# Optimization experiments

Measured on AMD Instinct MI355X. Metric: run time of the kernel, lower is better.

## Reference

```python
import jax, jax.numpy as jnp
import numpy as np

B, S, H = 2, 2048, 1024
NQ, NKV, HD, RANK = 16, 4, 64, 8
THETA = 10000.0
LORA_SCALE = 16 / RANK  # alpha / rank = 2.0
ATTN_SCALE = 1.0 / np.sqrt(HD)


def setup_inputs() -> dict:
    key = jax.random.key(0)
    ks = jax.random.split(key, 14)
    n = lambda k, shape, s: jax.random.normal(k, shape, jnp.float32) * s
    return {
        "x": n(ks[0], (B, S, H), 1.0),
        # nn.Linear weights: [out_features, in_features], y = x @ W.T (scaled small for stability)
        "Wq": n(ks[1], (NQ * HD, H), 0.02),
        "Wk": n(ks[2], (NKV * HD, H), 0.02),
        "Wv": n(ks[3], (NKV * HD, H), 0.02),
        "Wo": n(ks[4], (H, NQ * HD), 0.02),
        "qA": n(ks[5], (RANK, H), 0.05), "qB": n(ks[6], (NQ * HD, RANK), 0.05),
        "kA": n(ks[7], (RANK, H), 0.05), "kB": n(ks[8], (NKV * HD, RANK), 0.05),
        "vA": n(ks[9], (RANK, H), 0.05), "vB": n(ks[10], (NKV * HD, RANK), 0.05),
        "oA": n(ks[11], (RANK, NQ * HD), 0.05), "oB": n(ks[12], (H, RANK), 0.05),
    }


def _lora_proj(x, W, A, Bm):
    # x @ W.T + ((x @ A.T) @ B.T) * lora_scaling
    return x @ W.T + ((x @ A.T) @ Bm.T) * LORA_SCALE


def _rope(x, cos_h, sin_h):
    # x: [b, h, s, d]; even/odd interleaved split, concatenated output (matches torch ref)
    x1, x2 = x[..., ::2], x[..., 1::2]
    return jnp.concatenate([x1 * cos_h - x2 * sin_h, x1 * sin_h + x2 * cos_h], axis=-1)


def _forward(x, Wq, Wk, Wv, Wo, qA, qB, kA, kB, vA, vB, oA, oB):
    b, s, _ = x.shape
    q = _lora_proj(x, Wq, qA, qB).reshape(b, s, NQ, HD).transpose(0, 2, 1, 3)
    k = _lora_proj(x, Wk, kA, kB).reshape(b, s, NKV, HD).transpose(0, 2, 1, 3)
    v = _lora_proj(x, Wv, vA, vB).reshape(b, s, NKV, HD).transpose(0, 2, 1, 3)

    inv_freq = 1.0 / (THETA ** (jnp.arange(0, HD, 2, dtype=jnp.float32) / HD))  # [HD/2]
    freqs = jnp.arange(s, dtype=jnp.float32)[:, None] * inv_freq[None, :]  # [s, HD/2]
    cos_h = jnp.cos(freqs)[None, None]  # [1,1,s,HD/2]
    sin_h = jnp.sin(freqs)[None, None]
    q = _rope(q, cos_h, sin_h)
    k = _rope(k, cos_h, sin_h)

    rep = NQ // NKV  # GQA: repeat_interleave along head axis
    k = jnp.repeat(k, rep, axis=1)
    v = jnp.repeat(v, rep, axis=1)

    attn = jax.nn.softmax(jnp.einsum('bhqd,bhkd->bhqk', q, k) * ATTN_SCALE, axis=-1)
    out = jnp.einsum('bhqk,bhkd->bhqd', attn, v)
    out = out.transpose(0, 2, 1, 3).reshape(b, s, NQ * HD)
    return _lora_proj(out, Wo, oA, oB)


def reference(x, Wq, Wk, Wv, Wo, qA, qB, kA, kB, vA, vB, oA, oB):
    return _forward(x, Wq, Wk, Wv, Wo, qA, qB, kA, kB, vA, vB, oA, oB)
```

## Files before the change

### kernel.cpp

```cpp
#include <hip/hip_runtime.h>

typedef _Float16 f16;
typedef __attribute__((ext_vector_type(8))) _Float16 f16x8;
typedef __attribute__((ext_vector_type(4))) float f32x4;

#define DI __device__ __forceinline__
#define MFMA16(a, b, c) __builtin_amdgcn_mfma_f32_16x16x32_f16(a, b, c, 0, 0, 0)

constexpr int BB = 2, SS = 2048, HH = 1024;
constexpr int NQ = 16, NKV = 4, HD = 64;
constexpr int NTOK = BB * SS;
constexpr int NQKV = NQ*HD + 2*NKV*HD;

DI f32x4 zero4() { f32x4 z = {0.f, 0.f, 0.f, 0.f}; return z; }

DI float fexp2(float x) {
#if __has_builtin(__builtin_amdgcn_exp2f)
  return __builtin_amdgcn_exp2f(x);
#else
  return exp2f(x);
#endif
}

DI void glds16(const void* g, void* l) {
  __builtin_amdgcn_global_load_lds((const __attribute__((address_space(1))) void*)g,
                                   (__attribute__((address_space(3))) void*)l, 16, 0, 0);
}

DI int shuf32(int i) {
  return (i & ~31) | (((i >> 2) & 3) << 3) | (i & 3) | (((i >> 4) & 1) << 2);
}

__global__ __launch_bounds__(256) void prep_kernel(
    const float* __restrict__ x,
    const float* __restrict__ Wq, const float* __restrict__ Wk,
    const float* __restrict__ Wv, const float* __restrict__ Wo,
    const float* __restrict__ qA, const float* __restrict__ qB,
    const float* __restrict__ kA, const float* __restrict__ kB,
    const float* __restrict__ vA, const float* __restrict__ vB,
    const float* __restrict__ oA, const float* __restrict__ oB,
    f16* __restrict__ xh, f16* __restrict__ Wqkv, f16* __restrict__ Woe,
    float* __restrict__ ctab, float* __restrict__ stab) {
  int idx = blockIdx.x * 256 + threadIdx.x;
  if (idx < NQKV * HH) {
    int n = idx >> 10, hcol = idx & 1023;
    const float *Am, *Bm; float wv; int nn;
    if (n < 1024)      { nn = n;        wv = Wq[idx];              Am = qA; Bm = qB; }
    else if (n < 1280) { nn = n - 1024; wv = Wk[nn*1024 + hcol];   Am = kA; Bm = kB; }
    else               { nn = n - 1280; wv = Wv[nn*1024 + hcol];   Am = vA; Bm = vB; }
    float s = 0.f;
#pragma unroll
    for (int r = 0; r < 8; ++r) s += Bm[nn*8 + r] * Am[r*1024 + hcol];
    Wqkv[shuf32(idx)] = (f16)(wv + 2.0f * s);
  } else if ((idx -= NQKV * HH) < 1024 * 1024) {
    int n = idx >> 10, hcol = idx & 1023;
    float s = 0.f;
#pragma unroll
    for (int r = 0; r < 8; ++r) s += oB[n*8 + r] * oA[r*1024 + hcol];
    Woe[shuf32(idx)] = (f16)(Wo[idx] + 2.0f * s);
  } else if ((idx -= 1024 * 1024) < NTOK * HH) {
    xh[shuf32(idx)] = (f16)x[idx];
  } else if ((idx -= NTOK * HH) < SS * 32) {
    int s = idx >> 5, d = idx & 31;
    float inv = expf(-(float)d * 0.28782313662425583f);
    float ang = (float)s * inv;
    ctab[idx] = cosf(ang);
    stab[idx] = sinf(ang);
  }
}

template<typename OUT_T>
__global__ __launch_bounds__(256, 2) void gemm_bt(const f16* __restrict__ A, const f16* __restrict__ Bw,
                                                  OUT_T* __restrict__ C, int M, int N, int K) {
  __shared__ char lds[65536];
  const int nt = N >> 7;
  const int nwg = (M >> 7) * nt;
  int bid = blockIdx.x;
  const int cpx = nwg >> 3;
  bid = (bid & 7) * cpx + (bid >> 3);
  const int m0 = (bid / nt) << 7;
  const int n0 = (bid % nt) << 7;
  const int tid = threadIdx.x;
  const int lane = tid & 63;
  const int w = tid >> 6, wr = w >> 1, wc = w & 1;
  const int l15 = lane & 15, g = (lane >> 4) & 3;
  const char* Ab = (const char*)A;
  const char* Bb = (const char*)Bw;
  const size_t Kb = (size_t)K * 2;
  const int srow = tid >> 3;
  const int scol = (tid & 7) << 4;

  auto stage = [&](int kt, int bs) {
    char* ab = lds + bs * 32768;
    char* bbuf = ab + 16384;
    const size_t kbyte = (size_t)kt << 7;
#pragma unroll
    for (int s = 0; s < 4; ++s) {
      int row = (s << 5) + srow;
      glds16(Ab + (size_t)(m0 + row) * Kb + kbyte + (scol ^ ((row & 7) << 4)),
             ab + (s << 12) + (w << 10));
    }
#pragma unroll
    for (int s = 0; s < 4; ++s) {
      int row = (s << 5) + srow;
      glds16(Bb + (size_t)(n0 + row) * Kb + kbyte + (scol ^ ((row & 7) << 4)),
             bbuf + (s << 12) + (w << 10));
    }
  };

  f32x4 acc[4][4];
#pragma unroll
  for (int i = 0; i < 4; ++i)
#pragma unroll
    for (int j = 0; j < 4; ++j) acc[i][j] = zero4();

  const int nkt = K >> 6;
  stage(0, 0);
  for (int t = 0; t < nkt; ++t) {
    __syncthreads();
    if (t + 1 < nkt) stage(t + 1, (t + 1) & 1);
    const char* ab = lds + (t & 1) * 32768;
    const char* bbuf = ab + 16384;
    f16x8 af[4][2], bf[4][2];
#pragma unroll
    for (int mi = 0; mi < 4; ++mi) {
      int ra = (wr << 6) + (mi << 4) + l15;
      int base = ra << 7, sw = (ra & 7) << 4;
#pragma unroll
      for (int kk = 0; kk < 2; ++kk)
        af[mi][kk] = *reinterpret_cast<const f16x8*>(ab + base + ((((kk << 6) + (g << 4))) ^ sw));
    }
#pragma unroll
    for (int nj = 0; nj < 4; ++nj) {
      int rb = (wc << 6) + (nj << 4) + l15;
      int base = rb << 7, sw = (rb & 7) << 4;
#pragma unroll
      for (int kk = 0; kk < 2; ++kk)
        bf[nj][kk] = *reinterpret_cast<const f16x8*>(bbuf + base + ((((kk << 6) + (g << 4))) ^ sw));
    }
#pragma unroll
    for (int mi = 0; mi < 4; ++mi)
#pragma unroll
      for (int nj = 0; nj < 4; ++nj) {
        acc[mi][nj] = MFMA16(af[mi][0], bf[nj][0], acc[mi][nj]);
        acc[mi][nj] = MFMA16(af[mi][1], bf[nj][1], acc[mi][nj]);
      }
  }
#pragma unroll
  for (int mi = 0; mi < 4; ++mi)
#pragma unroll
    for (int nj = 0; nj < 4; ++nj) {
      int mmb = m0 + (wr << 6) + (mi << 4) + (g << 2);
      int nn  = n0 + (wc << 6) + (nj << 4) + l15;
      f32x4 a = acc[mi][nj];
#pragma unroll
      for (int r = 0; r < 4; ++r) C[(size_t)(mmb + r) * N + nn] = (OUT_T)a[r];
    }
}

__global__ __launch_bounds__(256) void rope_kernel(const f16* __restrict__ qkv,
    const float* __restrict__ ctab, const float* __restrict__ stab,
    f16* __restrict__ Qr, f16* __restrict__ Kr) {
  int idx = blockIdx.x * 256 + threadIdx.x;
  int dp = idx & 31;
  int t = idx >> 5;
  int hh = t % 20;
  int tok = t / 20;
  int s = tok & (SS - 1), b = tok >> 11;
  float c  = ctab[(s << 5) + dp];
  float sn = stab[(s << 5) + dp];
  const f16* row = qkv + (size_t)tok * NQKV;
  int p1 = (((dp >> 2) & 3) << 3) | (dp & 3) | (((dp >> 4) & 1) << 2);
  if (hh < 16) {
    float x1 = (float)row[hh*64 + 2*dp], x2 = (float)row[hh*64 + 2*dp + 1];
    f16* out = Qr + ((size_t)(b*NQ + hh)*SS + s) * HD;
    constexpr float QS = 0.18033688011112042f;
    out[p1]      = (f16)(QS * (x1*c  - x2*sn));
    out[p1 + 32] = (f16)(QS * (x1*sn + x2*c));
  } else {
    int hk = hh - 16;
    float x1 = (float)row[1024 + hk*64 + 2*dp], x2 = (float)row[1024 + hk*64 + 2*dp + 1];
    f16* out = Kr + ((size_t)(b*NKV + hk)*SS + s) * HD;
    out[p1]      = (f16)(x1*c  - x2*sn);
    out[p1 + 32] = (f16)(x1*sn + x2*c);
  }
}

__global__ __launch_bounds__(256) void vtrans_kernel(const f16* __restrict__ qkv,
                                                     f16* __restrict__ Vt) {
  __shared__ f16 Ls[64 * 72];
  const int tid = threadIdx.x;
  const int blk = blockIdx.x;
  const int st = blk & 31, hkv = (blk >> 5) & 3, b = blk >> 7;
  const int s0 = st << 6;
  {
    int s = tid >> 2, d0 = (tid & 3) << 4;
    const f16* src = qkv + ((size_t)(b*SS + s0 + s)) * NQKV + 1280 + hkv*64 + d0;
    uint4 v0 = *reinterpret_cast<const uint4*>(src);
    uint4 v1 = *reinterpret_cast<const uint4*>(src + 8);
    *reinterpret_cast<uint4*>(Ls + s * 72 + d0) = v0;
    *reinterpret_cast<uint4*>(Ls + s * 72 + d0 + 8) = v1;
  }
  __syncthreads();
  int d = tid >> 2;
  f16* dst = Vt + ((size_t)(b*NKV + hkv)*64 + d) * SS + s0;
#pragma unroll
  for (int cc = 0; cc < 2; ++cc) {
    int cch = ((tid & 3) << 1) + cc;
    int m = cch >> 2, g = cch & 3;
    union { f16 h[8]; uint4 u; } o;
#pragma unroll
    for (int j = 0; j < 8; ++j) {
      int sl = (m << 5) + (g << 2) + (j & 3) + ((j >> 2) << 4);
      o.h[j] = Ls[sl * 72 + d];
    }
    *reinterpret_cast<uint4*>(dst + (cch << 3)) = o.u;
  }
}

__global__ __launch_bounds__(256, 2) void attn_kernel(
    const f16* __restrict__ Qr, const f16* __restrict__ Kr,
    const f16* __restrict__ Vt, f16* __restrict__ AO) {
  __shared__ f16 smem[2 * 16384];
  const int tid = threadIdx.x, lane = tid & 63, w = tid >> 6;
  const int l15 = lane & 15, g = (lane >> 4) & 3;
  const int bh = blockIdx.x;
  const int b = bh >> 4, h = bh & 15, hkv = h >> 2;
  const int q0 = blockIdx.y << 7;
  const char* Kbase = (const char*)(Kr + (size_t)(b*NKV + hkv) * SS * HD);
  const char* Vbase = (const char*)(Vt + (size_t)(b*NKV + hkv) * HD * SS);

  f16x8 qf[2][2];
  {
    const f16* qr0 = Qr + ((size_t)(b*NQ + h)*SS + q0 + (w << 5) + l15) * HD + (g << 3);
    qf[0][0] = *reinterpret_cast<const f16x8*>(qr0);
    qf[0][1] = *reinterpret_cast<const f16x8*>(qr0 + 32);
    qf[1][0] = *reinterpret_cast<const f16x8*>(qr0 + 16*HD);
    qf[1][1] = *reinterpret_cast<const f16x8*>(qr0 + 16*HD + 32);
  }
  f16x8 ones;
#pragma unroll
  for (int i = 0; i < 8; ++i) ones[i] = (f16)1.0f;
  const f32x4 minit = {-4.f, -4.f, -4.f, -4.f};

  f32x4 acc[4][2];
#pragma unroll
  for (int i = 0; i < 4; ++i) { acc[i][0] = zero4(); acc[i][1] = zero4(); }
  f32x4 es0 = zero4(), es1 = zero4();

  auto stage = [&](int kv0, int bs) {
    char* kb = (char*)smem + bs * 32768;
    char* vb = kb + 16384;
#pragma unroll
    for (int s = 0; s < 4; ++s) {
      int L = (s << 12) + (tid << 4);
      int row = L >> 7, colb = L & 127;
      glds16(Kbase + (size_t)(kv0 + row) * 128 + (colb ^ ((row & 7) << 4)),
             kb + (s << 12) + (w << 10));
    }
#pragma unroll
    for (int s = 0; s < 4; ++s) {
      int L = (s << 12) + (tid << 4);
      int row = L >> 8, colb = L & 255;
      glds16(Vbase + (size_t)row * 4096 + (kv0 << 1) + (colb ^ ((row & 7) << 4)),
             vb + (s << 12) + (w << 10));
    }
  };

  stage(0, 0);

  for (int t = 0; t < 16; ++t) {
    __syncthreads();
    if (t < 15) stage((t + 1) << 7, (t + 1) & 1);
    const char* kb = (const char*)smem + (t & 1) * 32768;
    const char* vb = kb + 16384;

    f32x4 sf[2][8];
    __builtin_amdgcn_s_setprio(1);
#pragma unroll
    for (int mb = 0; mb < 8; ++mb) {
      int rowK = (mb << 4) + l15;
      int Bk = (rowK << 7) + ((g << 4) ^ ((rowK & 7) << 4));
      f16x8 kf0 = *reinterpret_cast<const f16x8*>(kb + Bk);
      f16x8 kf1 = *reinterpret_cast<const f16x8*>(kb + (Bk ^ 64));
      f32x4 z0 = minit, z1 = minit;
      z0 = MFMA16(kf0, qf[0][0], z0); z0 = MFMA16(kf1, qf[0][1], z0);
      z1 = MFMA16(kf0, qf[1][0], z1); z1 = MFMA16(kf1, qf[1][1], z1);
      sf[0][mb] = z0; sf[1][mb] = z1;
    }
    __builtin_amdgcn_s_setprio(0);
    union { f16 hv[32]; f16x8 v[4]; } p0, p1;
#pragma unroll
    for (int mb = 0; mb < 8; ++mb)
#pragma unroll
      for (int r = 0; r < 4; ++r) {
        p0.hv[(mb << 2) + r] = (f16)fexp2(sf[0][mb][r]);
        p1.hv[(mb << 2) + r] = (f16)fexp2(sf[1][mb][r]);
      }
    __builtin_amdgcn_s_setprio(1);
#pragma unroll
    for (int db = 0; db < 4; ++db) {
      int rowV = (db << 4) + l15;
      int Bv = (rowV << 8) + ((g << 4) ^ ((rowV & 7) << 4));
      f32x4 a0 = acc[db][0], a1 = acc[db][1];
#pragma unroll
      for (int sh = 0; sh < 4; ++sh) {
        f16x8 vf = *reinterpret_cast<const f16x8*>(vb + (Bv ^ (sh << 6)));
        a0 = MFMA16(vf, p0.v[sh], a0);
        a1 = MFMA16(vf, p1.v[sh], a1);
      }
      acc[db][0] = a0; acc[db][1] = a1;
    }
#pragma unroll
    for (int sh = 0; sh < 4; ++sh) {
      es0 = MFMA16(ones, p0.v[sh], es0);
      es1 = MFMA16(ones, p1.v[sh], es1);
    }
    __builtin_amdgcn_s_setprio(0);
  }
  float i0 = 1.0f / es0[0], i1 = 1.0f / es1[0];
  int sg0 = q0 + (w << 5) + l15;
  size_t ob0 = ((size_t)b * SS + sg0) * 1024 + h * 64;
  size_t ob1 = ob0 + (size_t)16 * 1024;
#pragma unroll
  for (int db = 0; db < 4; ++db) {
    union { f16 hv[4]; uint2 u; } o0, o1;
#pragma unroll
    for (int r = 0; r < 4; ++r) {
      o0.hv[r] = (f16)(acc[db][0][r] * i0);
      o1.hv[r] = (f16)(acc[db][1][r] * i1);
    }
    int pos = ((db >> 1) << 5) + (g << 3) + ((db & 1) << 2);
    *reinterpret_cast<uint2*>(AO + ob0 + pos) = o0.u;
    *reinterpret_cast<uint2*>(AO + ob1 + pos) = o1.u;
  }
}

extern "C" void kernel_launch(void* const* d_in, const int* in_sizes, int n_in,
                              void* d_out, int out_size, void* d_ws, size_t ws_size,
                              hipStream_t stream) {
  const float* x  = (const float*)d_in[0];
  const float* Wq = (const float*)d_in[1];
  const float* Wk = (const float*)d_in[2];
  const float* Wv = (const float*)d_in[3];
  const float* Wo = (const float*)d_in[4];
  const float* qA = (const float*)d_in[5];
  const float* qB = (const float*)d_in[6];
  const float* kA = (const float*)d_in[7];
  const float* kB = (const float*)d_in[8];
  const float* vA = (const float*)d_in[9];
  const float* vB = (const float*)d_in[10];
  const float* oA = (const float*)d_in[11];
  const float* oB = (const float*)d_in[12];
  char* ws = (char*)d_ws;
  f16* xh    = (f16*)(ws);
  f16* Wqkv  = (f16*)(ws + 8388608);
  f16* Woe   = (f16*)(ws + 11534336);
  f16* qkv   = (f16*)(ws + 13631488);
  f16* Qr    = (f16*)(ws + 26214400);
  f16* Kr    = (f16*)(ws + 34603008);
  f16* Vt    = (f16*)(ws + 36700160);
  float* ctab = (float*)(ws + 38797312);
  float* stab = (float*)(ws + 39059456);
  f16* AO = xh;
  float* out = (float*)d_out;

  prep_kernel<<<26880, 256, 0, stream>>>(x, Wq, Wk, Wv, Wo, qA, qB, kA, kB, vA, vB, oA, oB,
                                         xh, Wqkv, Woe, ctab, stab);
  gemm_bt<f16><<<dim3(32 * 12), 256, 0, stream>>>(xh, Wqkv, qkv, 4096, 1536, 1024);
  rope_kernel<<<10240, 256, 0, stream>>>(qkv, ctab, stab, Qr, Kr);
  vtrans_kernel<<<256, 256, 0, stream>>>(qkv, Vt);
  attn_kernel<<<dim3(32, 16), 256, 0, stream>>>(Qr, Kr, Vt, AO);
  gemm_bt<float><<<dim3(32 * 8), 256, 0, stream>>>(AO, Woe, out, 4096, 1024, 1024);
}
```

Measured before the change: 96.44 us.

## Triple-buffer attention KV tiles with 64-key stages and partial vmcnt waits

The attention kernel's KV loop moves from double-buffered 128-key tiles to triple-buffered 64-key tiles, prefetching two stages ahead. It replaces __syncthreads with an explicit vmcnt(4) wait plus s_barrier so loads for the next tile stay in flight during compute. The exp results are also packed into f16 pairs with cvt_pkrtz, which rounds toward zero instead of to nearest. Per-iteration LDS use shrinks, which lowers register pressure for the score tile, but the loop now runs twice as many iterations and barriers.

```diff
diff --git a/kernel.cpp b/kernel.cpp
--- a/kernel.cpp
+++ b/kernel.cpp
@@ -19,6 +19,18 @@
   return __builtin_amdgcn_exp2f(x);
 #else
   return exp2f(x);
+#endif
+}
+
+DI unsigned pk2(float a, float b) {
+#if __has_builtin(__builtin_amdgcn_cvt_pkrtz)
+  typedef __fp16 fp16v2 __attribute__((ext_vector_type(2)));
+  union { fp16v2 h; unsigned u; } c;
+  c.h = __builtin_amdgcn_cvt_pkrtz(a, b);
+  return c.u;
+#else
+  union { f16 h[2]; unsigned u; } c;
+  c.h[0] = (f16)a; c.h[1] = (f16)b; return c.u;
 #endif
 }
 
@@ -221,7 +233,7 @@
 __global__ __launch_bounds__(256, 2) void attn_kernel(
     const f16* __restrict__ Qr, const f16* __restrict__ Kr,
     const f16* __restrict__ Vt, f16* __restrict__ AO) {
-  __shared__ f16 smem[2 * 16384];
+  __shared__ char lds[3 * 16384];
   const int tid = threadIdx.x, lane = tid & 63, w = tid >> 6;
   const int l15 = lane & 15, g = (lane >> 4) & 3;
   const int bh = blockIdx.x;
@@ -248,37 +260,40 @@
   for (int i = 0; i < 4; ++i) { acc[i][0] = zero4(); acc[i][1] = zero4(); }
   f32x4 es0 = zero4(), es1 = zero4();
 
-  auto stage = [&](int kv0, int bs) {
-    char* kb = (char*)smem + bs * 32768;
-    char* vb = kb + 16384;
-#pragma unroll
-    for (int s = 0; s < 4; ++s) {
-      int L = (s << 12) + (tid << 4);
-      int row = L >> 7, colb = L & 127;
-      glds16(Kbase + (size_t)(kv0 + row) * 128 + (colb ^ ((row & 7) << 4)),
+  const int srow = tid >> 3;
+  const int scolb = (tid & 7) << 4;
+  auto stage = [&](int kv0, int buf) {
+    char* kb = lds + buf * 16384;
+    char* vb = kb + 8192;
+#pragma unroll
+    for (int s = 0; s < 2; ++s) {
+      int row = (s << 5) + srow;
+      glds16(Kbase + (size_t)(kv0 + row) * 128 + (scolb ^ ((row & 7) << 4)),
              kb + (s << 12) + (w << 10));
-    }
-#pragma unroll
-    for (int s = 0; s < 4; ++s) {
-      int L = (s << 12) + (tid << 4);
-      int row = L >> 8, colb = L & 255;
-      glds16(Vbase + (size_t)row * 4096 + (kv0 << 1) + (colb ^ ((row & 7) << 4)),
+      glds16(Vbase + (size_t)row * 4096 + (kv0 << 1) + (scolb ^ ((row & 7) << 4)),
              vb + (s << 12) + (w << 10));
     }
   };
 
   stage(0, 0);
-
-  for (int t = 0; t < 16; ++t) {
-    __syncthreads();
-    if (t < 15) stage((t + 1) << 7, (t + 1) & 1);
-    const char* kb = (const char*)smem + (t & 1) * 32768;
-    const char* vb = kb + 16384;
-
-    f32x4 sf[2][8];
+  stage(64, 1);
+  int cur = 0;
+
+  for (int t = 0; t < 32; ++t) {
+    if (t < 31) asm volatile("s_waitcnt vmcnt(4)" ::: "memory");
+    else        asm volatile("s_waitcnt vmcnt(0)" ::: "memory");
+    __builtin_amdgcn_s_barrier();
+    __builtin_amdgcn_sched_barrier(0);
+    int nb = cur + 2; if (nb >= 3) nb -= 3;
+    if (t + 2 < 32) stage((t + 2) << 6, nb);
+
+    const char* kb = lds + cur * 16384;
+    const char* vb = kb + 8192;
+
+    f32x4 sf0[4], sf1[4];
     __builtin_amdgcn_s_setprio(1);
 #pragma unroll
-    for (int mb = 0; mb < 8; ++mb) {
+    for (int mb = 0; mb < 4; ++mb) {
       int rowK = (mb << 4) + l15;
       int Bk = (rowK << 7) + ((g << 4) ^ ((rowK & 7) << 4));
       f16x8 kf0 = *reinterpret_cast<const f16x8*>(kb + Bk);
@@ -286,38 +301,37 @@
       f32x4 z0 = minit, z1 = minit;
       z0 = MFMA16(kf0, qf[0][0], z0); z0 = MFMA16(kf1, qf[0][1], z0);
       z1 = MFMA16(kf0, qf[1][0], z1); z1 = MFMA16(kf1, qf[1][1], z1);
-      sf[0][mb] = z0; sf[1][mb] = z1;
+      sf0[mb] = z0; sf1[mb] = z1;
     }
     __builtin_amdgcn_s_setprio(0);
-    union { f16 hv[32]; f16x8 v[4]; } p0, p1;
-#pragma unroll
-    for (int mb = 0; mb < 8; ++mb)
-#pragma unroll
-      for (int r = 0; r < 4; ++r) {
-        p0.hv[(mb << 2) + r] = (f16)fexp2(sf[0][mb][r]);
-        p1.hv[(mb << 2) + r] = (f16)fexp2(sf[1][mb][r]);
+
+    union { unsigned u[8]; f16x8 v[2]; } p0, p1;
+#pragma unroll
+    for (int j = 0; j < 8; ++j) {
+      int mb = j >> 1, r0 = (j & 1) << 1;
+      p0.u[j] = pk2(fexp2(sf0[mb][r0]), fexp2(sf0[mb][r0 + 1]));
+      p1.u[j] = pk2(fexp2(sf1[mb][r0]), fexp2(sf1[mb][r0 + 1]));
+    }
+
+    __builtin_amdgcn_s_setprio(1);
+#pragma unroll
+    for (int sh = 0; sh < 2; ++sh) {
+#pragma unroll
+      for (int db = 0; db < 4; ++db) {
+        int rowV = (db << 4) + l15;
+        int Bv = (rowV << 7) + ((g << 4) ^ ((rowV & 7) << 4));
+        f16x8 vf = *reinterpret_cast<const f16x8*>(vb + (Bv ^ (sh << 6)));
+        acc[db][0] = MFMA16(vf, p0.v[sh], acc[db][0]);
+        acc[db][1] = MFMA16(vf, p1.v[sh], acc[db][1]);
       }
-    __builtin_amdgcn_s_setprio(1);
-#pragma unroll
-    for (int db = 0; db < 4; ++db) {
-      int rowV = (db << 4) + l15;
-      int Bv = (rowV << 8) + ((g << 4) ^ ((rowV & 7) << 4));
-      f32x4 a0 = acc[db][0], a1 = acc[db][1];
-#pragma unroll
-      for (int sh = 0; sh < 4; ++sh) {
-        f16x8 vf = *reinterpret_cast<const f16x8*>(vb + (Bv ^ (sh << 6)));
-        a0 = MFMA16(vf, p0.v[sh], a0);
-        a1 = MFMA16(vf, p1.v[sh], a1);
-      }
-      acc[db][0] = a0; acc[db][1] = a1;
-    }
-#pragma unroll
-    for (int sh = 0; sh < 4; ++sh) {
       es0 = MFMA16(ones, p0.v[sh], es0);
       es1 = MFMA16(ones, p1.v[sh], es1);
     }
     __builtin_amdgcn_s_setprio(0);
-  }
+
+    cur += 1; if (cur == 3) cur = 0;
+  }
+
   float i0 = 1.0f / es0[0], i1 = 1.0f / es1[0];
   int sg0 = q0 + (w << 5) + l15;
   size_t ob0 = ((size_t)b * SS + sg0) * 1024 + h * 64;
```

Measured after the change: 96.15 us. About the same (-0.3%).
